# Optimization experiments

Measured on AMD Instinct MI355X. Metric: run time of the kernel, lower is better.

The kernel has to match this reference:

```python
import jax, jax.numpy as jnp
import numpy as np

B, T, D = 4, 2048, 1024
H, Dh = 16, 64


def setup_inputs() -> dict:
    key = jax.random.key(0)
    ks = jax.random.split(key, 5)
    # kaiming_normal_ on [H, Dh, D]: fan_in = Dh*D (torch default fan_in over dims[1:]),
    # std = sqrt(2/fan_in); exact init distribution does not affect correctness checks.
    std_qkv = float(np.sqrt(2.0 / (Dh * D)))
    std_o = float(np.sqrt(2.0 / (D * Dh)))
    return {
        "x": jax.random.normal(ks[0], (B, T, D), dtype=jnp.float32),
        "W_Q": jax.random.normal(ks[1], (H, Dh, D), dtype=jnp.float32) * std_qkv,
        "b_Q": jnp.zeros((H, Dh), dtype=jnp.float32),
        "W_K": jax.random.normal(ks[2], (H, Dh, D), dtype=jnp.float32) * std_qkv,
        "b_K": jnp.zeros((H, Dh), dtype=jnp.float32),
        "W_V": jax.random.normal(ks[3], (H, Dh, D), dtype=jnp.float32) * std_qkv,
        "b_V": jnp.zeros((H, Dh), dtype=jnp.float32),
        "W_O": jax.random.normal(ks[4], (H, D, Dh), dtype=jnp.float32) * std_o,
        "b_O": jnp.zeros((D,), dtype=jnp.float32),
    }


def reference(x, W_Q, b_Q, W_K, b_K, W_V, b_V, W_O, b_O):
    # Q/K/V: [batch, tok, heads, d_head]
    Q = jnp.einsum("btd,hkd->bthk", x, W_Q) + b_Q
    K = jnp.einsum("btd,hkd->bthk", x, W_K) + b_K
    V = jnp.einsum("btd,hkd->bthk", x, W_V) + b_V
    d_head = W_Q.shape[1]
    # scores: [batch, heads, tok_Q, tok_K]
    scores = jnp.einsum("bqhk,bshk->bhqs", Q, K) / jnp.sqrt(jnp.asarray(d_head, x.dtype))
    attn = jax.nn.softmax(scores, axis=-1)
    # out per head: [batch, tok_Q, heads, d_head]
    out_h = jnp.einsum("bhqs,bshk->bqhk", attn, V)
    # project back: [batch, tok, d_model]
    return jnp.einsum("bqhk,hdk->bqd", out_h, W_O) + b_O
```

## Files before the change

### kernel.cpp

```cpp
#include <hip/hip_runtime.h>
#include <stdint.h>


typedef __attribute__((ext_vector_type(8))) short bf16x8;
typedef __attribute__((ext_vector_type(4))) float f32x4;

#define MFMA32 __builtin_amdgcn_mfma_f32_16x16x32_bf16

#if __has_builtin(__builtin_amdgcn_exp2f)
#define EXP2(x) __builtin_amdgcn_exp2f(x)
#else
#define EXP2(x) exp2f(x)
#endif

__device__ __forceinline__ unsigned short f2bf(float f) {
  union { float f; unsigned int u; } v; v.f = f;
  unsigned int r = v.u + 0x7FFFu + ((v.u >> 16) & 1u);
  return (unsigned short)(r >> 16);
}

__device__ __forceinline__ void gl_lds16(const void* g, void* l) {
  __builtin_amdgcn_global_load_lds(
      (const __attribute__((address_space(1))) unsigned int*)g,
      (__attribute__((address_space(3))) unsigned int*)l, 16, 0, 0);
}

__device__ __forceinline__ unsigned packbf2(float lo, float hi) {
  union { float f; unsigned u; } a, b; a.f = lo; b.f = hi;
  return __builtin_amdgcn_perm(b.u, a.u, 0x07060302u);
}

__device__ __forceinline__ int rho(int r) { return (r & 3) | ((r >> 1) & 4); }

__device__ __forceinline__ void conv8(const float* __restrict__ src,
                                      unsigned short* __restrict__ dst, int i) {
  const float4* sp = (const float4*)src;
  float4 a = sp[2 * i], b = sp[2 * i + 1];
  union { unsigned short u[8]; uint4 v; } o;
  o.u[0] = f2bf(a.x); o.u[1] = f2bf(a.y); o.u[2] = f2bf(a.z); o.u[3] = f2bf(a.w);
  o.u[4] = f2bf(b.x); o.u[5] = f2bf(b.y); o.u[6] = f2bf(b.z); o.u[7] = f2bf(b.w);
  ((uint4*)dst)[i] = o.v;
}

__global__ __launch_bounds__(256) void prep_all(
    const float* __restrict__ x, const float* __restrict__ WQ,
    const float* __restrict__ WK, const float* __restrict__ WV,
    const float* __restrict__ WO, unsigned short* __restrict__ Xb,
    unsigned short* __restrict__ Wqkv, unsigned short* __restrict__ Wot) {
  const int bx = blockIdx.x, t = threadIdx.x;
  if (bx < 4096) {
    conv8(x, Xb, bx * 256 + t);
  } else if (bx < 4608) {
    conv8(WQ, Wqkv, (bx - 4096) * 256 + t);
  } else if (bx < 5120) {
    conv8(WK, Wqkv + 1048576, (bx - 4608) * 256 + t);
  } else if (bx < 5632) {
    conv8(WV, Wqkv + 2097152, (bx - 5120) * 256 + t);
  } else {
    int tid = (bx - 5632) * 256 + t;
    int h = tid >> 13, rem = tid & 8191;
    int d = rem >> 3, c = rem & 7;
    const float4* sp = (const float4*)(WO + (size_t)h * 65536 + d * 64 + c * 8);
    float4 a = sp[0], e = sp[1];
    union { unsigned short u[8]; uint4 v; } o;
    o.u[0] = f2bf(a.x); o.u[1] = f2bf(a.y); o.u[2] = f2bf(a.z); o.u[3] = f2bf(a.w);
    o.u[4] = f2bf(e.x); o.u[5] = f2bf(e.y); o.u[6] = f2bf(e.z); o.u[7] = f2bf(e.w);
    *(uint4*)(Wot + (size_t)d * 1024 + h * 64 + c * 8) = o.v;
  }
}


template <int MH, int C>
__device__ __forceinline__ void qkv_ds_a(const unsigned short* A, int wm, int quad,
                                         int l15, bf16x8 ar[4][2]) {
#pragma unroll
  for (int ii = 0; ii < 4; ++ii) {
    int ra = wm * 128 + MH * 64 + ii * 16 + l15;
    ar[ii][C] = *(const bf16x8*)(A + ra * 64 + (((C * 4 + quad) ^ (ra & 7)) * 8));
  }
}

template <int C>
__device__ __forceinline__ void qkv_ds_b(const unsigned short* B, int wn, int quad,
                                         int l15, bf16x8 br[3][2]) {
#pragma unroll
  for (int nj = 0; nj < 3; ++nj) {
    int rb = wn * 48 + nj * 16 + l15;
    br[nj][C] = *(const bf16x8*)(B + rb * 64 + (((C * 4 + quad) ^ (rb & 7)) * 8));
  }
}

template <int MH, int C>
__device__ __forceinline__ void qkv_mf(const bf16x8 ar[4][2], const bf16x8 br[3][2],
                                       f32x4 acc[8][3]) {
#pragma unroll
  for (int ii = 0; ii < 4; ++ii)
#pragma unroll
    for (int nj = 0; nj < 3; ++nj)
      acc[MH * 4 + ii][nj] =
          MFMA32(ar[ii][C], br[nj][C], acc[MH * 4 + ii][nj], 0, 0, 0);
}

#define QKV_BAR() __builtin_amdgcn_s_barrier()
#define QKV_LGKM0() asm volatile("s_waitcnt lgkmcnt(0)" ::: "memory")
#define SA_(bb, kt, u) \
  gl_lds16(Xb + (size_t)aoff[u] + (size_t)(kt) * 64, lds + (bb)*28672 + adst[u])
#define SB_(bb, kt, u) \
  gl_lds16(Wqkv + (size_t)boff[u] + (size_t)(kt) * 64, lds + (bb)*28672 + 16384 + bdst[u])

__global__ __launch_bounds__(512, 2) void gemm_qkv(
    const unsigned short* __restrict__ Xb, const unsigned short* __restrict__ Wqkv,
    const float* __restrict__ bQ, const float* __restrict__ bK,
    const float* __restrict__ bV, unsigned short* __restrict__ Qg,
    unsigned short* __restrict__ Kg, unsigned int* __restrict__ Vpg) {
  __shared__ unsigned short lds[57344];
  const int tid = threadIdx.x, lane = tid & 63, w = tid >> 6;
  const int quad = lane >> 4, l15 = lane & 15;
  const int wm = w >> 2, wn = w & 3;
  const int m0 = blockIdx.x * 256, n0 = blockIdx.y * 192;

  int aoff[4], adst[4];
#pragma unroll
  for (int u = 0; u < 4; ++u) {
    int s = u * 512 + tid, row = s >> 3;
    aoff[u] = (m0 + row) * 1024 + (((s & 7) ^ (row & 7)) * 8);
    adst[u] = s * 8;
  }
  int boff[3], bdst[3];
#pragma unroll
  for (int u = 0; u < 3; ++u) {
    int s = u * 512 + tid, row = s >> 3;
    boff[u] = (n0 + row) * 1024 + (((s & 7) ^ (row & 7)) * 8);
    bdst[u] = s * 8;
  }

  const unsigned short* A0 = lds;
  const unsigned short* B0 = lds + 16384;
  const unsigned short* A1 = lds + 28672;
  const unsigned short* B1 = lds + 45056;

  f32x4 acc[8][3];
#pragma unroll
  for (int i = 0; i < 8; ++i)
#pragma unroll
    for (int j = 0; j < 3; ++j) acc[i][j] = (f32x4){0.f, 0.f, 0.f, 0.f};
  bf16x8 ar[4][2], br[3][2];

  SA_(0, 0, 0); SA_(0, 0, 1); SA_(0, 0, 2); SA_(0, 0, 3);
  SB_(0, 0, 0); SB_(0, 0, 1); SB_(0, 0, 2);
  SB_(1, 1, 0); SB_(1, 1, 1); SB_(1, 1, 2);
  asm volatile("s_waitcnt vmcnt(3)" ::: "memory");
  QKV_BAR();

#pragma unroll 1
  for (int i = 0; i < 8; ++i) {
    const int tn = 2 * i + 2;
    const bool st = (i < 7);
    qkv_ds_a<0, 0>(A0, wm, quad, l15, ar);
    qkv_ds_b<0>(B0, wn, quad, l15, br);
    SA_(1, 2 * i + 1, 0); SA_(1, 2 * i + 1, 1);
    QKV_BAR(); QKV_LGKM0();
    __builtin_amdgcn_s_setprio(1); qkv_mf<0, 0>(ar, br, acc); __builtin_amdgcn_s_setprio(0);
    QKV_BAR();
    qkv_ds_a<0, 1>(A0, wm, quad, l15, ar);
    qkv_ds_b<1>(B0, wn, quad, l15, br);
    SA_(1, 2 * i + 1, 2); SA_(1, 2 * i + 1, 3);
    QKV_BAR(); QKV_LGKM0();
    __builtin_amdgcn_s_setprio(1); qkv_mf<0, 1>(ar, br, acc); __builtin_amdgcn_s_setprio(0);
    QKV_BAR();
    qkv_ds_a<1, 0>(A0, wm, quad, l15, ar);
    if (st) { SB_(0, tn, 0); SB_(0, tn, 1); }
    QKV_BAR(); QKV_LGKM0();
    __builtin_amdgcn_s_setprio(1); qkv_mf<1, 0>(ar, br, acc); __builtin_amdgcn_s_setprio(0);
    QKV_BAR();
    qkv_ds_a<1, 1>(A0, wm, quad, l15, ar);
    if (st) SB_(0, tn, 2);
    QKV_BAR(); QKV_LGKM0();
    __builtin_amdgcn_s_setprio(1); qkv_mf<1, 1>(ar, br, acc); __builtin_amdgcn_s_setprio(0);
    if (st) asm volatile("s_waitcnt vmcnt(3)" ::: "memory");
    else    asm volatile("s_waitcnt vmcnt(0)" ::: "memory");
    QKV_BAR();
    qkv_ds_a<0, 0>(A1, wm, quad, l15, ar);
    qkv_ds_b<0>(B1, wn, quad, l15, br);
    if (st) { SA_(0, tn, 0); SA_(0, tn, 1); }
    QKV_BAR(); QKV_LGKM0();
    __builtin_amdgcn_s_setprio(1); qkv_mf<0, 0>(ar, br, acc); __builtin_amdgcn_s_setprio(0);
    QKV_BAR();
    qkv_ds_a<0, 1>(A1, wm, quad, l15, ar);
    qkv_ds_b<1>(B1, wn, quad, l15, br);
    if (st) { SA_(0, tn, 2); SA_(0, tn, 3); }
    QKV_BAR(); QKV_LGKM0();
    __builtin_amdgcn_s_setprio(1); qkv_mf<0, 1>(ar, br, acc); __builtin_amdgcn_s_setprio(0);
    QKV_BAR();
    qkv_ds_a<1, 0>(A1, wm, quad, l15, ar);
    if (st) { SB_(1, tn + 1, 0); SB_(1, tn + 1, 1); }
    QKV_BAR(); QKV_LGKM0();
    __builtin_amdgcn_s_setprio(1); qkv_mf<1, 0>(ar, br, acc); __builtin_amdgcn_s_setprio(0);
    QKV_BAR();
    qkv_ds_a<1, 1>(A1, wm, quad, l15, ar);
    if (st) SB_(1, tn + 1, 2);
    QKV_BAR(); QKV_LGKM0();
    __builtin_amdgcn_s_setprio(1); qkv_mf<1, 1>(ar, br, acc); __builtin_amdgcn_s_setprio(0);
    asm volatile("s_waitcnt vmcnt(3)" ::: "memory");
    QKV_BAR();
  }

#pragma unroll
  for (int nj = 0; nj < 3; ++nj) {
    const int n_abs = n0 + wn * 48 + nj * 16 + l15;
    const int type = n_abs >> 10;
    const int n_in = n_abs & 1023;
    const int h = n_in >> 6, kh = n_in & 63;
    const float bv = ((type == 0) ? bQ : (type == 1) ? bK : bV)[n_in];
#pragma unroll
    for (int mi = 0; mi < 8; ++mi) {
      const int mb = m0 + wm * 128 + mi * 16 + quad * 4;
      const int b = mb >> 11, tb = mb & 2047;
      if (type == 2) {
        uint2 pk;
        pk.x = (unsigned)f2bf(acc[mi][nj][0] + bv) |
               ((unsigned)f2bf(acc[mi][nj][1] + bv) << 16);
        pk.y = (unsigned)f2bf(acc[mi][nj][2] + bv) |
               ((unsigned)f2bf(acc[mi][nj][3] + bv) << 16);
        *(uint2*)(Vpg + ((size_t)(b * 16 + h) * 64 + kh) * 1024 + (tb >> 1)) = pk;
      } else {
        unsigned short* dst =
            ((type == 0) ? Qg : Kg) + ((size_t)(b * 16 + h) * 2048 + tb) * 64 + kh;
        const float sc = (type == 0) ? 0.18033688011112042f : 1.0f;
        dst[0]   = f2bf((acc[mi][nj][0] + bv) * sc);
        dst[64]  = f2bf((acc[mi][nj][1] + bv) * sc);
        dst[128] = f2bf((acc[mi][nj][2] + bv) * sc);
        dst[192] = f2bf((acc[mi][nj][3] + bv) * sc);
      }
    }
  }
}

#undef SA_
#undef SB_
#undef QKV_BAR
#undef QKV_LGKM0

__device__ __forceinline__ void stage_kv(const unsigned short* __restrict__ Kb,
                                         const unsigned int* __restrict__ Vb,
                                         unsigned short* smem, int tid, int s0, int b) {
#pragma unroll
  for (int u = 0; u < 2; ++u) {
    int s = u * 256 + tid, row = s >> 3, g = (s & 7) ^ rho(row);
    gl_lds16(Kb + (size_t)(s0 + row) * 64 + g * 8, smem + b * 8192 + s * 8);
    gl_lds16(Vb + (size_t)row * 1024 + (s0 >> 1) + g * 4,
             smem + b * 8192 + 4096 + s * 8);
  }
}

__global__ __launch_bounds__(256, 2) void flash_attn(
    const unsigned short* __restrict__ Qg, const unsigned short* __restrict__ Kg,
    const unsigned int* __restrict__ Vpg, unsigned short* __restrict__ OH) {
  __shared__ unsigned short smem[16384];
  const int tid = threadIdx.x, lane = tid & 63, w = tid >> 6;
  const int quad = lane >> 4, l15 = lane & 15;
  const int bh = blockIdx.x, qt = blockIdx.y;

  const unsigned short* Qb = Qg + ((size_t)bh * 2048 + qt * 256) * 64;
  const unsigned short* Kb = Kg + (size_t)bh * 2048 * 64;
  const unsigned int*  Vb = Vpg + (size_t)bh * 64 * 1024;

#pragma unroll
  for (int u = 0; u < 8; ++u) {
    int s = u * 256 + tid, row = s >> 3;
    gl_lds16(Qb + row * 64 + ((s & 7) ^ (row & 7)) * 8, smem + s * 8);
  }
  __syncthreads();

  bf16x8 qf[4][2];
#pragma unroll
  for (int qi = 0; qi < 4; ++qi) {
    int row = w * 64 + qi * 16 + l15;
#pragma unroll
    for (int c = 0; c < 2; ++c)
      qf[qi][c] = *(const bf16x8*)(smem + row * 64 + (((c * 4 + quad) ^ (row & 7)) * 8));
  }
  __syncthreads();

  stage_kv(Kb, Vb, smem, tid, 0, 0);

  union { uint4 q; bf16x8 v; } onesu;
  onesu.q = make_uint4(0x3F803F80u, 0x3F803F80u, 0x3F803F80u, 0x3F803F80u);
  const bf16x8 ones = onesu.v;

  f32x4 o[4][4];
  f32x4 lacc[4];
#pragma unroll
  for (int qi = 0; qi < 4; ++qi) {
    lacc[qi] = (f32x4){0.f, 0.f, 0.f, 0.f};
#pragma unroll
    for (int nj = 0; nj < 4; ++nj) o[qi][nj] = (f32x4){0.f, 0.f, 0.f, 0.f};
  }

  for (int t = 0; t < 32; ++t) {
    __syncthreads();
    if (t < 31) stage_kv(Kb, Vb, smem, tid, (t + 1) * 64, (t + 1) & 1);
    const unsigned short* Kd = smem + (t & 1) * 8192;
    const unsigned short* Vd = Kd + 4096;

#pragma unroll
    for (int blk = 0; blk < 2; ++blk) {
      bf16x8 vb[4];
#pragma unroll
      for (int nj = 0; nj < 4; ++nj) {
        int vrow = nj * 16 + l15;
        vb[nj] = *(const bf16x8*)(Vd + vrow * 64 + (((blk * 4 + quad) ^ rho(vrow)) * 8));
      }
      union { unsigned u[4]; bf16x8 v; } pa[4];
#pragma unroll
      for (int v = 0; v < 2; ++v) {
        int krow = blk * 32 + 8 * (l15 >> 2) + 4 * v + (l15 & 3);
        const unsigned short* kr = Kd + krow * 64;
        bf16x8 ka0 = *(const bf16x8*)(kr + ((quad ^ rho(krow)) * 8));
        bf16x8 ka1 = *(const bf16x8*)(kr + (((4 + quad) ^ rho(krow)) * 8));
#pragma unroll
        for (int qi = 0; qi < 4; ++qi) {
          f32x4 S = (f32x4){0.f, 0.f, 0.f, 0.f};
          S = MFMA32(ka0, qf[qi][0], S, 0, 0, 0);
          S = MFMA32(ka1, qf[qi][1], S, 0, 0, 0);
          float e0 = EXP2(S[0]), e1 = EXP2(S[1]), e2 = EXP2(S[2]), e3 = EXP2(S[3]);
          pa[qi].u[2 * v] = packbf2(e0, e1);
          pa[qi].u[2 * v + 1] = packbf2(e2, e3);
        }
      }
      __builtin_amdgcn_s_setprio(1);
#pragma unroll
      for (int qi = 0; qi < 4; ++qi) {
        lacc[qi] = MFMA32(pa[qi].v, ones, lacc[qi], 0, 0, 0);
#pragma unroll
        for (int nj = 0; nj < 4; ++nj)
          o[qi][nj] = MFMA32(pa[qi].v, vb[nj], o[qi][nj], 0, 0, 0);
      }
      __builtin_amdgcn_s_setprio(0);
    }
  }

  const int b = bh >> 4, h = bh & 15;
#pragma unroll
  for (int qi = 0; qi < 4; ++qi) {
#pragma unroll
    for (int r = 0; r < 4; ++r) {
      float lr = 1.0f / lacc[qi][r];
      int trow = qt * 256 + w * 64 + qi * 16 + 4 * quad + r;
#pragma unroll
      for (int nj = 0; nj < 4; ++nj) {
        int col = h * 64 + nj * 16 + l15;
        OH[((size_t)b * 2048 + trow) * 1024 + col] = f2bf(o[qi][nj][r] * lr);
      }
    }
  }
}

__global__ __launch_bounds__(256) void gemm_o(
    const unsigned short* __restrict__ OHm, const unsigned short* __restrict__ Wot,
    const float* __restrict__ bO, float* __restrict__ Out) {
  __shared__ unsigned short As[128 * 64];
  __shared__ unsigned short Bs[64 * 64];
  const int tid = threadIdx.x, lane = tid & 63, w = tid >> 6;
  const int quad = lane >> 4, l15 = lane & 15;
  const int wm = w & 1, wn = w >> 1;
  const int m0 = blockIdx.x * 128, n0 = blockIdx.y * 64;
  f32x4 acc[4][2];
#pragma unroll
  for (int i = 0; i < 4; ++i)
#pragma unroll
    for (int j = 0; j < 2; ++j) acc[i][j] = (f32x4){0.f, 0.f, 0.f, 0.f};

  for (int k0 = 0; k0 < 1024; k0 += 64) {
    __syncthreads();
#pragma unroll
    for (int u = 0; u < 4; ++u) {
      int s = u * 256 + tid, row = s >> 3;
      int cl = ((s & 7) ^ (row & 7)) * 8;
      gl_lds16(OHm + (size_t)(m0 + row) * 1024 + k0 + cl, As + s * 8);
    }
#pragma unroll
    for (int u = 0; u < 2; ++u) {
      int s = u * 256 + tid, row = s >> 3;
      int cl = ((s & 7) ^ (row & 7)) * 8;
      gl_lds16(Wot + (size_t)(n0 + row) * 1024 + k0 + cl, Bs + s * 8);
    }
    __syncthreads();
    bf16x8 af[4][2], bfr[2][2];
#pragma unroll
    for (int i = 0; i < 4; ++i) {
      int ra = wm * 64 + i * 16 + l15;
#pragma unroll
      for (int c = 0; c < 2; ++c)
        af[i][c] = *(const bf16x8*)(As + ra * 64 + (((c * 4 + quad) ^ (ra & 7)) * 8));
    }
#pragma unroll
    for (int j = 0; j < 2; ++j) {
      int rb = wn * 32 + j * 16 + l15;
#pragma unroll
      for (int c = 0; c < 2; ++c)
        bfr[j][c] = *(const bf16x8*)(Bs + rb * 64 + (((c * 4 + quad) ^ (rb & 7)) * 8));
    }
#pragma unroll
    for (int mi = 0; mi < 4; ++mi)
#pragma unroll
      for (int nj = 0; nj < 2; ++nj) {
        acc[mi][nj] = MFMA32(af[mi][0], bfr[nj][0], acc[mi][nj], 0, 0, 0);
        acc[mi][nj] = MFMA32(af[mi][1], bfr[nj][1], acc[mi][nj], 0, 0, 0);
      }
  }

#pragma unroll
  for (int nj = 0; nj < 2; ++nj) {
    const int n = n0 + wn * 32 + nj * 16 + l15;
    const float bv = bO[n];
#pragma unroll
    for (int mi = 0; mi < 4; ++mi) {
      const int mb = m0 + wm * 64 + mi * 16 + quad * 4;
#pragma unroll
      for (int r = 0; r < 4; ++r)
        Out[(size_t)(mb + r) * 1024 + n] = acc[mi][nj][r] + bv;
    }
  }
}

extern "C" void kernel_launch(void* const* d_in, const int* in_sizes, int n_in,
                              void* d_out, int out_size, void* d_ws, size_t ws_size,
                              hipStream_t stream) {
  const float* x  = (const float*)d_in[0];
  const float* WQ = (const float*)d_in[1];
  const float* bQ = (const float*)d_in[2];
  const float* WK = (const float*)d_in[3];
  const float* bK = (const float*)d_in[4];
  const float* WV = (const float*)d_in[5];
  const float* bV = (const float*)d_in[6];
  const float* WO = (const float*)d_in[7];
  const float* bO = (const float*)d_in[8];
  float* out = (float*)d_out;

  char* ws = (char*)d_ws;
  unsigned short* Xb   = (unsigned short*)(ws);
  unsigned short* OH   = (unsigned short*)(ws);
  unsigned short* Wqkv = (unsigned short*)(ws + 16777216);
  unsigned short* Wot  = (unsigned short*)(ws + 23068672);
  unsigned short* Qg   = (unsigned short*)(ws + 25165824);
  unsigned short* Kg   = (unsigned short*)(ws + 41943040);
  unsigned int*   Vpg  = (unsigned int*)  (ws + 58720256);

  prep_all<<<6144, 256, 0, stream>>>(x, WQ, WK, WV, WO, Xb, Wqkv, Wot);

  dim3 g1(32, 16);
  gemm_qkv<<<g1, 512, 0, stream>>>(Xb, Wqkv, bQ, bK, bV, Qg, Kg, Vpg);
  dim3 g2(64, 8);
  flash_attn<<<g2, 256, 0, stream>>>(Qg, Kg, Vpg, OH);
  dim3 g3(64, 16);
  gemm_o<<<g3, 256, 0, stream>>>(OH, Wot, bO, out);
}
```

Before: 255.1 us.

## Rewrite output projection GEMM with larger tiles and double-buffered pipelined loads

The output projection GEMM moves from a 128x64 tile with 256 threads and single-buffered LDS to a 256x128 tile with 512 threads and double-buffered LDS. Global-to-LDS loads for the next K tiles are interleaved with the MFMA phases, and the MFMA phases are wrapped in setprio, reusing the QKV GEMM's barrier and fragment-load helpers. The aim is to hide memory latency and raise data reuse per block. The cost is higher register and LDS pressure (96KB LDS per block) and only 256 blocks, which may leave parts of the device underfilled.

```diff
diff --git a/kernel.cpp b/kernel.cpp
--- a/kernel.cpp
+++ b/kernel.cpp
@@ -238,8 +238,6 @@
 
 #undef SA_
 #undef SB_
-#undef QKV_BAR
-#undef QKV_LGKM0
 
 __device__ __forceinline__ void stage_kv(const unsigned short* __restrict__ Kb,
                                          const unsigned int* __restrict__ Vb,
@@ -356,58 +354,126 @@
   }
 }
 
-__global__ __launch_bounds__(256) void gemm_o(
+
+template <int C>
+__device__ __forceinline__ void go_ds_b(const unsigned short* B, int wn, int quad,
+                                        int l15, bf16x8 br[2][2]) {
+#pragma unroll
+  for (int nj = 0; nj < 2; ++nj) {
+    int rb = wn * 32 + nj * 16 + l15;
+    br[nj][C] = *(const bf16x8*)(B + rb * 64 + (((C * 4 + quad) ^ (rb & 7)) * 8));
+  }
+}
+
+template <int MH, int C>
+__device__ __forceinline__ void go_mf(const bf16x8 ar[4][2], const bf16x8 br[2][2],
+                                      f32x4 acc[8][2]) {
+#pragma unroll
+  for (int ii = 0; ii < 4; ++ii)
+#pragma unroll
+    for (int nj = 0; nj < 2; ++nj)
+      acc[MH * 4 + ii][nj] =
+          MFMA32(ar[ii][C], br[nj][C], acc[MH * 4 + ii][nj], 0, 0, 0);
+}
+
+#define SA_(bb, kt, u) \
+  gl_lds16(OHm + (size_t)aoff[u] + (size_t)(kt) * 64, lds + (bb)*24576 + adst[u])
+#define SB_(bb, kt, u) \
+  gl_lds16(Wot + (size_t)boff[u] + (size_t)(kt) * 64, lds + (bb)*24576 + 16384 + bdst[u])
+
+__global__ __launch_bounds__(512, 2) void gemm_o(
     const unsigned short* __restrict__ OHm, const unsigned short* __restrict__ Wot,
     const float* __restrict__ bO, float* __restrict__ Out) {
-  __shared__ unsigned short As[128 * 64];
-  __shared__ unsigned short Bs[64 * 64];
+  __shared__ unsigned short lds[49152];
   const int tid = threadIdx.x, lane = tid & 63, w = tid >> 6;
   const int quad = lane >> 4, l15 = lane & 15;
-  const int wm = w & 1, wn = w >> 1;
-  const int m0 = blockIdx.x * 128, n0 = blockIdx.y * 64;
-  f32x4 acc[4][2];
-#pragma unroll
-  for (int i = 0; i < 4; ++i)
+  const int wm = w >> 2, wn = w & 3;
+  const int m0 = blockIdx.x * 256, n0 = blockIdx.y * 128;
+
+  int aoff[4], adst[4];
+#pragma unroll
+  for (int u = 0; u < 4; ++u) {
+    int s = u * 512 + tid, row = s >> 3;
+    aoff[u] = (m0 + row) * 1024 + (((s & 7) ^ (row & 7)) * 8);
+    adst[u] = s * 8;
+  }
+  int boff[2], bdst[2];
+#pragma unroll
+  for (int u = 0; u < 2; ++u) {
+    int s = u * 512 + tid, row = s >> 3;
+    boff[u] = (n0 + row) * 1024 + (((s & 7) ^ (row & 7)) * 8);
+    bdst[u] = s * 8;
+  }
+
+  const unsigned short* A0 = lds;
+  const unsigned short* B0 = lds + 16384;
+  const unsigned short* A1 = lds + 24576;
+  const unsigned short* B1 = lds + 40960;
+
+  f32x4 acc[8][2];
+#pragma unroll
+  for (int i = 0; i < 8; ++i)
 #pragma unroll
     for (int j = 0; j < 2; ++j) acc[i][j] = (f32x4){0.f, 0.f, 0.f, 0.f};
-
-  for (int k0 = 0; k0 < 1024; k0 += 64) {
-    __syncthreads();
-#pragma unroll
-    for (int u = 0; u < 4; ++u) {
-      int s = u * 256 + tid, row = s >> 3;
-      int cl = ((s & 7) ^ (row & 7)) * 8;
-      gl_lds16(OHm + (size_t)(m0 + row) * 1024 + k0 + cl, As + s * 8);
-    }
-#pragma unroll
-    for (int u = 0; u < 2; ++u) {
-      int s = u * 256 + tid, row = s >> 3;
-      int cl = ((s & 7) ^ (row & 7)) * 8;
-      gl_lds16(Wot + (size_t)(n0 + row) * 1024 + k0 + cl, Bs + s * 8);
-    }
-    __syncthreads();
-    bf16x8 af[4][2], bfr[2][2];
-#pragma unroll
-    for (int i = 0; i < 4; ++i) {
-      int ra = wm * 64 + i * 16 + l15;
-#pragma unroll
-      for (int c = 0; c < 2; ++c)
-        af[i][c] = *(const bf16x8*)(As + ra * 64 + (((c * 4 + quad) ^ (ra & 7)) * 8));
-    }
-#pragma unroll
-    for (int j = 0; j < 2; ++j) {
-      int rb = wn * 32 + j * 16 + l15;
-#pragma unroll
-      for (int c = 0; c < 2; ++c)
-        bfr[j][c] = *(const bf16x8*)(Bs + rb * 64 + (((c * 4 + quad) ^ (rb & 7)) * 8));
-    }
-#pragma unroll
-    for (int mi = 0; mi < 4; ++mi)
-#pragma unroll
-      for (int nj = 0; nj < 2; ++nj) {
-        acc[mi][nj] = MFMA32(af[mi][0], bfr[nj][0], acc[mi][nj], 0, 0, 0);
-        acc[mi][nj] = MFMA32(af[mi][1], bfr[nj][1], acc[mi][nj], 0, 0, 0);
-      }
+  bf16x8 ar[4][2], br[2][2];
+
+  SA_(0, 0, 0); SA_(0, 0, 1); SA_(0, 0, 2); SA_(0, 0, 3);
+  SB_(0, 0, 0); SB_(0, 0, 1);
+  SB_(1, 1, 0); SB_(1, 1, 1);
+  asm volatile("s_waitcnt vmcnt(2)" ::: "memory");
+  QKV_BAR();
+
+#pragma unroll 1
+  for (int i = 0; i < 8; ++i) {
+    const int tn = 2 * i + 2;
+    const bool st = (i < 7);
+    qkv_ds_a<0, 0>(A0, wm, quad, l15, ar);
+    go_ds_b<0>(B0, wn, quad, l15, br);
+    SA_(1, 2 * i + 1, 0); SA_(1, 2 * i + 1, 1);
+    QKV_BAR(); QKV_LGKM0();
+    __builtin_amdgcn_s_setprio(1); go_mf<0, 0>(ar, br, acc); __builtin_amdgcn_s_setprio(0);
+    QKV_BAR();
+    qkv_ds_a<0, 1>(A0, wm, quad, l15, ar);
+    go_ds_b<1>(B0, wn, quad, l15, br);
+    SA_(1, 2 * i + 1, 2); SA_(1, 2 * i + 1, 3);
+    QKV_BAR(); QKV_LGKM0();
+    __builtin_amdgcn_s_setprio(1); go_mf<0, 1>(ar, br, acc); __builtin_amdgcn_s_setprio(0);
+    QKV_BAR();
+    qkv_ds_a<1, 0>(A0, wm, quad, l15, ar);
+    if (st) SB_(0, tn, 0);
+    QKV_BAR(); QKV_LGKM0();
+    __builtin_amdgcn_s_setprio(1); go_mf<1, 0>(ar, br, acc); __builtin_amdgcn_s_setprio(0);
+    QKV_BAR();
+    qkv_ds_a<1, 1>(A0, wm, quad, l15, ar);
+    if (st) SB_(0, tn, 1);
+    QKV_BAR(); QKV_LGKM0();
+    __builtin_amdgcn_s_setprio(1); go_mf<1, 1>(ar, br, acc); __builtin_amdgcn_s_setprio(0);
+    if (st) asm volatile("s_waitcnt vmcnt(2)" ::: "memory");
+    else    asm volatile("s_waitcnt vmcnt(0)" ::: "memory");
+    QKV_BAR();
+    qkv_ds_a<0, 0>(A1, wm, quad, l15, ar);
+    go_ds_b<0>(B1, wn, quad, l15, br);
+    if (st) { SA_(0, tn, 0); SA_(0, tn, 1); }
+    QKV_BAR(); QKV_LGKM0();
+    __builtin_amdgcn_s_setprio(1); go_mf<0, 0>(ar, br, acc); __builtin_amdgcn_s_setprio(0);
+    QKV_BAR();
+    qkv_ds_a<0, 1>(A1, wm, quad, l15, ar);
+    go_ds_b<1>(B1, wn, quad, l15, br);
+    if (st) { SA_(0, tn, 2); SA_(0, tn, 3); }
+    QKV_BAR(); QKV_LGKM0();
+    __builtin_amdgcn_s_setprio(1); go_mf<0, 1>(ar, br, acc); __builtin_amdgcn_s_setprio(0);
+    QKV_BAR();
+    qkv_ds_a<1, 0>(A1, wm, quad, l15, ar);
+    if (st) SB_(1, tn + 1, 0);
+    QKV_BAR(); QKV_LGKM0();
+    __builtin_amdgcn_s_setprio(1); go_mf<1, 0>(ar, br, acc); __builtin_amdgcn_s_setprio(0);
+    QKV_BAR();
+    qkv_ds_a<1, 1>(A1, wm, quad, l15, ar);
+    if (st) SB_(1, tn + 1, 1);
+    QKV_BAR(); QKV_LGKM0();
+    __builtin_amdgcn_s_setprio(1); go_mf<1, 1>(ar, br, acc); __builtin_amdgcn_s_setprio(0);
+    asm volatile("s_waitcnt vmcnt(2)" ::: "memory");
+    QKV_BAR();
   }
 
 #pragma unroll
@@ -415,14 +481,19 @@
     const int n = n0 + wn * 32 + nj * 16 + l15;
     const float bv = bO[n];
 #pragma unroll
-    for (int mi = 0; mi < 4; ++mi) {
-      const int mb = m0 + wm * 64 + mi * 16 + quad * 4;
+    for (int mi = 0; mi < 8; ++mi) {
+      const int mb = m0 + wm * 128 + mi * 16 + quad * 4;
 #pragma unroll
       for (int r = 0; r < 4; ++r)
         Out[(size_t)(mb + r) * 1024 + n] = acc[mi][nj][r] + bv;
     }
   }
 }
+
+#undef SA_
+#undef SB_
+#undef QKV_BAR
+#undef QKV_LGKM0
 
 extern "C" void kernel_launch(void* const* d_in, const int* in_sizes, int n_in,
                               void* d_out, int out_size, void* d_ws, size_t ws_size,
@@ -453,6 +524,6 @@
   gemm_qkv<<<g1, 512, 0, stream>>>(Xb, Wqkv, bQ, bK, bV, Qg, Kg, Vpg);
   dim3 g2(64, 8);
   flash_attn<<<g2, 256, 0, stream>>>(Qg, Kg, Vpg, OH);
-  dim3 g3(64, 16);
-  gemm_o<<<g3, 256, 0, stream>>>(OH, Wot, bO, out);
-}
+  dim3 g3(32, 8);
+  gemm_o<<<g3, 512, 0, stream>>>(OH, Wot, bO, out);
+}
```

New measurement: 252.3 us. No clear change (-1.1%).
